# Performance work log

Hardware: AMD Instinct MI355X
Metric: run time of the kernel (lower is better)

Reference implementation:

```python
import jax, jax.numpy as jnp
import numpy as np

L, B, S, E, H, FF = 4, 1, 2048, 768, 12, 3072
DH = E // H
EPS = 1e-5

def setup_inputs() -> dict:
    key = jax.random.key(0)
    ks = jax.random.split(key, 10)
    w = lambda k, shape: jax.random.normal(k, shape, jnp.float32) * 0.02
    return {
        "inputs_embeds": jax.random.normal(ks[0], (B, S, E), jnp.float32),
        "wpe": w(ks[1], (S, E)),
        "ln1_g": jnp.ones((L, E), jnp.float32), "ln1_b": jnp.zeros((L, E), jnp.float32),
        "Wq": w(ks[2], (L, E, E)), "bq": jnp.zeros((L, E), jnp.float32),
        "Wk": w(ks[3], (L, E, E)), "bk": jnp.zeros((L, E), jnp.float32),
        "Wv": w(ks[4], (L, E, E)), "bv": jnp.zeros((L, E), jnp.float32),
        "Wo": w(ks[5], (L, E, E)), "bo": jnp.zeros((L, E), jnp.float32),
        "ln2_g": jnp.ones((L, E), jnp.float32), "ln2_b": jnp.zeros((L, E), jnp.float32),
        "W1": w(ks[6], (L, E, FF)), "b1": jnp.zeros((L, FF), jnp.float32),
        "W2": w(ks[7], (L, FF, E)), "b2": jnp.zeros((L, E), jnp.float32),
        "lnf_g": jnp.ones((E,), jnp.float32), "lnf_b": jnp.zeros((E,), jnp.float32),
    }

def _layernorm(x, g, b):
    mu = jnp.mean(x, axis=-1, keepdims=True)
    var = jnp.mean(jnp.square(x - mu), axis=-1, keepdims=True)
    return (x - mu) * jax.lax.rsqrt(var + EPS) * g + b

def _block(x, p):
    (g1, b1_, wq, bq, wk, bk, wv, bv, wo, bo, g2, b2_, w1, bb1, w2, bb2) = p
    h = _layernorm(x, g1, b1_)
    Bq, Sq, _ = x.shape
    q = (h @ wq + bq).reshape(Bq, Sq, H, DH)
    k = (h @ wk + bk).reshape(Bq, Sq, H, DH)
    v = (h @ wv + bv).reshape(Bq, Sq, H, DH)
    scale = DH ** (-0.5)
    # no softmax: purely linear scale * Q K^T V (attn_weights unused downstream)
    attn_w = jnp.einsum('bqhd,bkhd->bhqk', q, k) * scale  # [B,H,S,S]
    a = jnp.einsum('bhqk,bkhd->bqhd', attn_w, v).reshape(Bq, Sq, E)
    x = x + (a @ wo + bo)
    h2 = _layernorm(x, g2, b2_)
    mlp = jax.nn.gelu(h2 @ w1 + bb1, approximate=False) @ w2 + bb2
    return x + mlp

def reference(inputs_embeds, wpe, ln1_g, ln1_b, Wq, bq, Wk, bk, Wv, bv, Wo, bo,
              ln2_g, ln2_b, W1, b1, W2, b2, lnf_g, lnf_b):
    seq = inputs_embeds.shape[1]
    x = inputs_embeds + wpe[:seq]  # dropout p=0 -> identity
    layer_params = (ln1_g, ln1_b, Wq, bq, Wk, bk, Wv, bv, Wo, bo,
                    ln2_g, ln2_b, W1, b1, W2, b2)
    def body(carry, p):
        return _block(carry, p), None
    x, _ = jax.lax.scan(body, x, layer_params)
    return _layernorm(x, lnf_g, lnf_b)
```

## Files before the change

### kernel.cpp

```cpp
#include <hip/hip_runtime.h>
#include <hip/hip_bf16.h>
#include <math.h>

#define SS 2048
#define EE 768
#define HH 12
#define DHH 64
#define FFF 3072
#define LL 4

typedef __hip_bfloat16 bf16;
typedef __attribute__((ext_vector_type(8))) short short8;
typedef __attribute__((ext_vector_type(4))) float f32x4;

__device__ __forceinline__ float b2f(short u) {
  union { unsigned int i; float f; } v;
  v.i = ((unsigned int)(unsigned short)u) << 16;
  return v.f;
}
__device__ __forceinline__ bf16 f2b(float f) { return __float2bfloat16(f); }
__device__ __forceinline__ unsigned int f2bu(float f) {
  return (unsigned int)__bfloat16_as_ushort(__float2bfloat16(f));
}

__device__ __forceinline__ void async_ld16(const void* g, void* l) {
  __builtin_amdgcn_global_load_lds(
      (const __attribute__((address_space(1))) void*)g,
      (__attribute__((address_space(3))) void*)l, 16, 0, 0);
}

template <typename OutT>
__global__ __launch_bounds__(256) void ln_fused_kernel(
    float* x, const float* __restrict__ bias, const float* __restrict__ part,
    int nparts, const float* __restrict__ extra,
    const float* __restrict__ g, const float* __restrict__ bta,
    int writeback, int readx, OutT* __restrict__ out) {
  int row = blockIdx.x;
  int tid = threadIdx.x;
  float* xr = x + (size_t)row * EE;
  float v0 = 0.f, v1 = 0.f, v2 = 0.f;
  if (readx) { v0 = xr[tid]; v1 = xr[tid + 256]; v2 = xr[tid + 512]; }
  if (bias) { v0 += bias[tid]; v1 += bias[tid + 256]; v2 += bias[tid + 512]; }
  for (int p = 0; p < nparts; p++) {
    const float* pr = part + (size_t)p * SS * EE + (size_t)row * EE;
    v0 += pr[tid]; v1 += pr[tid + 256]; v2 += pr[tid + 512];
  }
  if (extra) {
    const float* er = extra + (size_t)row * EE;
    v0 += er[tid]; v1 += er[tid + 256]; v2 += er[tid + 512];
  }
  if (writeback) { xr[tid] = v0; xr[tid + 256] = v1; xr[tid + 512] = v2; }
  float s  = v0 + v1 + v2;
  float s2 = v0 * v0 + v1 * v1 + v2 * v2;
  #pragma unroll
  for (int off = 32; off >= 1; off >>= 1) {
    s  += __shfl_down(s,  off);
    s2 += __shfl_down(s2, off);
  }
  __shared__ float red[8];
  __shared__ float mb[2];
  int lane = tid & 63, wid = tid >> 6;
  if (lane == 0) { red[wid] = s; red[4 + wid] = s2; }
  __syncthreads();
  if (tid == 0) {
    float ts  = red[0] + red[1] + red[2] + red[3];
    float ts2 = red[4] + red[5] + red[6] + red[7];
    float mu  = ts * (1.0f / EE);
    float var = ts2 * (1.0f / EE) - mu * mu;
    mb[0] = mu; mb[1] = rsqrtf(var + 1e-5f);
  }
  __syncthreads();
  float mu = mb[0], rs = mb[1];
  OutT* orow = out + (size_t)row * EE;
  float o0 = (v0 - mu) * rs * g[tid]       + bta[tid];
  float o1 = (v1 - mu) * rs * g[tid + 256] + bta[tid + 256];
  float o2 = (v2 - mu) * rs * g[tid + 512] + bta[tid + 512];
  if constexpr (sizeof(OutT) == 4) {
    orow[tid] = o0; orow[tid + 256] = o1; orow[tid + 512] = o2;
  } else {
    orow[tid] = f2b(o0); orow[tid + 256] = f2b(o1); orow[tid + 512] = f2b(o2);
  }
}

__global__ __launch_bounds__(256) void transpose_all_kernel(
    const float* __restrict__ Wq, const float* __restrict__ Wk,
    const float* __restrict__ Wv, const float* __restrict__ Wo,
    const float* __restrict__ W1, const float* __restrict__ W2,
    bf16* __restrict__ WtAll) {
  __shared__ unsigned int lds[32][33];
  int bid = blockIdx.x;
  int l = bid / 3456, r = bid % 3456;
  bf16* base = WtAll + (size_t)l * 7077888;
  const float* src; bf16* dst; int K, N, rr;
  if (r < 864) {
    int m = r / 288; rr = r % 288;
    src = (m == 0 ? Wq : m == 1 ? Wk : Wv) + (size_t)l * EE * EE;
    dst = base + (size_t)m * 589824; K = 768; N = 768;
  } else if (r < 1152) {
    rr = r - 864; src = Wo + (size_t)l * EE * EE; dst = base + 1769472; K = 768; N = 768;
  } else if (r < 2304) {
    rr = r - 1152; src = W1 + (size_t)l * EE * FFF; dst = base + 2359296; K = 768; N = 3072;
  } else {
    rr = r - 2304; src = W2 + (size_t)l * FFF * EE; dst = base + 4718592; K = 3072; N = 768;
  }
  int ntn = N >> 5;
  int k0 = (rr / ntn) * 64, n0 = (rr % ntn) * 32;
  int tx = threadIdx.x & 31, ty = threadIdx.x >> 5;
  const float* s = src + (size_t)(k0 + ty * 8) * N + n0 + tx;
  #pragma unroll
  for (int j = 0; j < 4; j++) {
    float v0 = s[(size_t)(2 * j) * N];
    float v1 = s[(size_t)(2 * j + 1) * N];
    lds[tx][ty * 4 + j] = (f2bu(v1) << 16) | f2bu(v0);
  }
  __syncthreads();
  int n = threadIdx.x >> 3, kp4 = (threadIdx.x & 7) * 4;
  uint4 o;
  o.x = lds[n][kp4];     o.y = lds[n][kp4 + 1];
  o.z = lds[n][kp4 + 2]; o.w = lds[n][kp4 + 3];
  unsigned int* d = (unsigned int*)dst + (size_t)(n0 + n) * (K >> 1) + (k0 >> 1) + kp4;
  *(uint4*)d = o;
}

__global__ __launch_bounds__(256) void concat_bias_all_kernel(
    const float* __restrict__ bq, const float* __restrict__ bk,
    const float* __restrict__ bv, float* __restrict__ out) {
  int g = blockIdx.x * 256 + threadIdx.x;
  int l = g / 2304, i = g % 2304;
  out[g] = (i < 768) ? bq[l * 768 + i]
         : (i < 1536 ? bk[l * 768 + i - 768] : bv[l * 768 + i - 1536]);
}

__global__ __launch_bounds__(256) void gemm_bf16_kernel(
    const bf16* __restrict__ A, int lda, const bf16* __restrict__ Bt,
    const float* __restrict__ bias, void* __restrict__ Cv, void* __restrict__ Cv2,
    int K, int N, int mode) {
  __shared__ __align__(16) short As[64 * 64];
  __shared__ __align__(16) short Bs[64 * 64];
  const int t = threadIdx.x;
  const int wave = t >> 6, lane = t & 63;
  const int m0 = blockIdx.y * 64, n0 = blockIdx.x * 64;

  const int srow = t >> 3;
  const int sw   = (t & 7) ^ (srow & 7);
  const bf16* Ag = A  + (size_t)(m0 + srow) * lda + sw * 8;
  const bf16* Bg = Bt + (size_t)(n0 + srow) * K + sw * 8;

  const int fr = lane & 15, kq = lane >> 4;
  const int wm = (wave >> 1) * 32, wn = (wave & 1) * 32;
  f32x4 acc[2][2] = {};

  for (int k0 = 0; k0 < K; k0 += 64) {
    async_ld16(Ag + k0,                    As + wave * 512);
    async_ld16(Ag + (size_t)32 * lda + k0, As + 2048 + wave * 512);
    async_ld16(Bg + k0,                    Bs + wave * 512);
    async_ld16(Bg + (size_t)32 * K + k0,   Bs + 2048 + wave * 512);
    __syncthreads();
    #pragma unroll
    for (int s = 0; s < 2; s++) {
      short8 a[2], b[2];
      #pragma unroll
      for (int i = 0; i < 2; i++) {
        int r = wm + 16 * i + fr;
        int p = (kq + 4 * s) ^ (r & 7);
        a[i] = *(const short8*)(As + r * 64 + p * 8);
      }
      #pragma unroll
      for (int j = 0; j < 2; j++) {
        int r = wn + 16 * j + fr;
        int p = (kq + 4 * s) ^ (r & 7);
        b[j] = *(const short8*)(Bs + r * 64 + p * 8);
      }
      #pragma unroll
      for (int i = 0; i < 2; i++)
        #pragma unroll
        for (int j = 0; j < 2; j++)
          acc[i][j] = __builtin_amdgcn_mfma_f32_16x16x32_bf16(a[i], b[j], acc[i][j], 0, 0, 0);
    }
    __syncthreads();
  }

  #pragma unroll
  for (int i = 0; i < 2; i++) {
    #pragma unroll
    for (int j = 0; j < 2; j++) {
      const int r0 = m0 + wm + 16 * i + kq * 4;
      const int c  = n0 + wn + 16 * j + fr;
      const float bv = bias[c];
      if (mode == 4) {
        if (n0 < 768) {
          #pragma unroll
          for (int ri = 0; ri < 4; ri++)
            ((bf16*)Cv)[(size_t)(r0 + ri) * 768 + c] = f2b(acc[i][j][ri] + bv);
        } else {
          __align__(8) bf16 tb[4];
          #pragma unroll
          for (int ri = 0; ri < 4; ri++) tb[ri] = f2b(acc[i][j][ri] + bv);
          *(short4*)((short*)Cv2 + ((size_t)(c - 768) << 11) + r0) = *(short4*)&tb[0];
        }
      } else {
        #pragma unroll
        for (int ri = 0; ri < 4; ri++) {
          float val = acc[i][j][ri] + bv;
          val = 0.5f * val * (1.0f + erff(val * 0.70710678118654752f));
          ((bf16*)Cv)[(size_t)(r0 + ri) * N + c] = f2b(val);
        }
      }
    }
  }
}

__global__ __launch_bounds__(256) void gemm_resid_kernel(
    const bf16* __restrict__ A, int lda, const bf16* __restrict__ Bt,
    const float* __restrict__ bias, float* __restrict__ x,
    float* __restrict__ part, int K, int zsplit, int Ksplit) {
  __shared__ __align__(16) short As[64 * 64];
  __shared__ __align__(16) short Bs[64 * 64];
  const int t = threadIdx.x;
  const int wave = t >> 6, lane = t & 63;
  const int m0 = blockIdx.y * 64, n0 = blockIdx.x * 64;
  const int z = blockIdx.z;
  const int kBeg = z * Ksplit, kEnd = kBeg + Ksplit;

  const int srow = t >> 3;
  const int sw   = (t & 7) ^ (srow & 7);
  const bf16* Ag = A  + (size_t)(m0 + srow) * lda + sw * 8;
  const bf16* Bg = Bt + (size_t)(n0 + srow) * K + sw * 8;

  const int fr = lane & 15, kq = lane >> 4;
  const int wm = (wave >> 1) * 32, wn = (wave & 1) * 32;
  f32x4 acc[2][2] = {};

  for (int k0 = kBeg; k0 < kEnd; k0 += 64) {
    async_ld16(Ag + k0,                    As + wave * 512);
    async_ld16(Ag + (size_t)32 * lda + k0, As + 2048 + wave * 512);
    async_ld16(Bg + k0,                    Bs + wave * 512);
    async_ld16(Bg + (size_t)32 * K + k0,   Bs + 2048 + wave * 512);
    __syncthreads();
    #pragma unroll
    for (int s = 0; s < 2; s++) {
      short8 a[2], b[2];
      #pragma unroll
      for (int i = 0; i < 2; i++) {
        int r = wm + 16 * i + fr;
        int p = (kq + 4 * s) ^ (r & 7);
        a[i] = *(const short8*)(As + r * 64 + p * 8);
      }
      #pragma unroll
      for (int j = 0; j < 2; j++) {
        int r = wn + 16 * j + fr;
        int p = (kq + 4 * s) ^ (r & 7);
        b[j] = *(const short8*)(Bs + r * 64 + p * 8);
      }
      #pragma unroll
      for (int i = 0; i < 2; i++)
        #pragma unroll
        for (int j = 0; j < 2; j++)
          acc[i][j] = __builtin_amdgcn_mfma_f32_16x16x32_bf16(a[i], b[j], acc[i][j], 0, 0, 0);
    }
    __syncthreads();
  }

  #pragma unroll
  for (int i = 0; i < 2; i++) {
    #pragma unroll
    for (int j = 0; j < 2; j++) {
      const int r0 = m0 + wm + 16 * i + kq * 4;
      const int c  = n0 + wn + 16 * j + fr;
      if (zsplit > 1) {
        #pragma unroll
        for (int ri = 0; ri < 4; ri++)
          part[(size_t)z * SS * EE + (size_t)(r0 + ri) * EE + c] = acc[i][j][ri];
      } else {
        const float bv = bias[c];
        #pragma unroll
        for (int ri = 0; ri < 4; ri++) {
          const size_t idx = (size_t)(r0 + ri) * EE + c;
          x[idx] = acc[i][j][ri] + bv + x[idx];
        }
      }
    }
  }
}

__global__ __launch_bounds__(256) void attn_fused_kernel(
    const bf16* __restrict__ kvT, const bf16* __restrict__ Wo_t,
    bf16* __restrict__ Gt) {
  __shared__ short pbuf[4][4096];
  __shared__ short Ms[4096];
  const int nt = blockIdx.x, h = blockIdx.y;
  const int lane = threadIdx.x & 63, wave = threadIdx.x >> 6;
  const int fr = lane & 15, kq = lane >> 4;
  const short* kT = (const short*)kvT + (size_t)h * 64 * 2048;
  const short* vT = (const short*)kvT + (size_t)(768 + h * 64) * 2048;

  f32x4 acc[4][4] = {};
  for (int it = 0; it < 8; it++) {
    const int s0 = (it * 4 + wave) * 64;
    #pragma unroll
    for (int s = 0; s < 2; s++) {
      short8 a[4], b[4];
      #pragma unroll
      for (int i = 0; i < 4; i++)
        a[i] = *(const short8*)(kT + (size_t)(16 * i + fr) * 2048 + s0 + s * 32 + kq * 8);
      #pragma unroll
      for (int j = 0; j < 4; j++)
        b[j] = *(const short8*)(vT + (size_t)(16 * j + fr) * 2048 + s0 + s * 32 + kq * 8);
      #pragma unroll
      for (int i = 0; i < 4; i++)
        #pragma unroll
        for (int j = 0; j < 4; j++)
          acc[i][j] = __builtin_amdgcn_mfma_f32_16x16x32_bf16(a[i], b[j], acc[i][j], 0, 0, 0);
    }
  }
  #pragma unroll
  for (int i = 0; i < 4; i++)
    #pragma unroll
    for (int j = 0; j < 4; j++)
      #pragma unroll
      for (int ri = 0; ri < 4; ri++)
        pbuf[wave][(16 * i + kq * 4 + ri) * 64 + 16 * j + fr] =
            (short)__bfloat16_as_ushort(f2b(acc[i][j][ri]));
  __syncthreads();
  {
    int e0 = threadIdx.x * 16;
    #pragma unroll
    for (int e = 0; e < 16; e++) {
      float s = b2f(pbuf[0][e0 + e]) + b2f(pbuf[1][e0 + e]) +
                b2f(pbuf[2][e0 + e]) + b2f(pbuf[3][e0 + e]);
      Ms[e0 + e] = (short)__bfloat16_as_ushort(f2b(s * 0.125f));
    }
  }
  __syncthreads();

  const int nb = nt * 128 + wave * 32;
  f32x4 g[4][2] = {};
  #pragma unroll
  for (int s = 0; s < 2; s++) {
    short8 a[4], b[2];
    #pragma unroll
    for (int i = 0; i < 4; i++)
      a[i] = *(const short8*)(Ms + (16 * i + fr) * 64 + s * 32 + kq * 8);
    #pragma unroll
    for (int j = 0; j < 2; j++)
      b[j] = *(const short8*)((const short*)Wo_t +
             (size_t)(nb + 16 * j + fr) * 768 + h * 64 + s * 32 + kq * 8);
    #pragma unroll
    for (int i = 0; i < 4; i++)
      #pragma unroll
      for (int j = 0; j < 2; j++)
        g[i][j] = __builtin_amdgcn_mfma_f32_16x16x32_bf16(a[i], b[j], g[i][j], 0, 0, 0);
  }
  #pragma unroll
  for (int i = 0; i < 4; i++)
    #pragma unroll
    for (int j = 0; j < 2; j++) {
      const int c = nb + 16 * j + fr;
      const int d1 = 16 * i + kq * 4;
      __align__(8) bf16 tb[4];
      #pragma unroll
      for (int ri = 0; ri < 4; ri++) tb[ri] = f2b(g[i][j][ri]);
      *(short4*)((short*)Gt + (size_t)c * 768 + h * 64 + d1) = *(short4*)&tb[0];
    }
}

extern "C" void kernel_launch(void* const* d_in, const int* in_sizes, int n_in,
                              void* d_out, int out_size, void* d_ws, size_t ws_size,
                              hipStream_t stream) {
  const float* emb  = (const float*)d_in[0];
  const float* wpe  = (const float*)d_in[1];
  const float* ln1g = (const float*)d_in[2];
  const float* ln1b = (const float*)d_in[3];
  const float* Wq   = (const float*)d_in[4];
  const float* bq   = (const float*)d_in[5];
  const float* Wk   = (const float*)d_in[6];
  const float* bk   = (const float*)d_in[7];
  const float* Wv   = (const float*)d_in[8];
  const float* bv   = (const float*)d_in[9];
  const float* Wo   = (const float*)d_in[10];
  const float* bo   = (const float*)d_in[11];
  const float* ln2g = (const float*)d_in[12];
  const float* ln2b = (const float*)d_in[13];
  const float* W1   = (const float*)d_in[14];
  const float* b1   = (const float*)d_in[15];
  const float* W2   = (const float*)d_in[16];
  const float* b2   = (const float*)d_in[17];
  const float* lnfg = (const float*)d_in[18];
  const float* lnfb = (const float*)d_in[19];

  char* w = (char*)d_ws;
  bf16*  WtAll = (bf16*)w;   w += (size_t)4 * 7077888 * 2;
  float* bqkvA = (float*)w;  w += (size_t)4 * 2304 * 4;
  float* x     = (float*)w;  w += (size_t)SS * EE * 4;
  bf16*  hb    = (bf16*)w;   w += (size_t)SS * EE * 2;
  bf16*  qkvQ  = (bf16*)w;   w += (size_t)SS * EE * 2;
  bf16*  kvT   = (bf16*)w;   w += (size_t)1536 * 2048 * 2;
  bf16*  Gt    = (bf16*)w;   w += (size_t)EE * EE * 2;
  bf16*  mb2   = (bf16*)w;   w += (size_t)SS * FFF * 2;
  float* cpart = (float*)w;  w += (size_t)2 * SS * EE * 4;

  dim3 blk(256);
  transpose_all_kernel<<<13824, blk, 0, stream>>>(Wq, Wk, Wv, Wo, W1, W2, WtAll);
  concat_bias_all_kernel<<<36, blk, 0, stream>>>(bq, bk, bv, bqkvA);

  for (int l = 0; l < LL; l++) {
    bf16* Wl = WtAll + (size_t)l * 7077888;
    bf16* Wqkv_t = Wl;
    bf16* Wo_t   = Wl + 1769472;
    bf16* W1_t   = Wl + 2359296;
    bf16* W2_t   = Wl + 4718592;

    if (l == 0) {
      ln_fused_kernel<bf16><<<SS, blk, 0, stream>>>(
          x, nullptr, emb, 1, wpe, ln1g, ln1b, 1, 0, hb);
    } else {
      ln_fused_kernel<bf16><<<SS, blk, 0, stream>>>(
          x, b2 + (l - 1) * EE, cpart, 2, nullptr,
          ln1g + l * EE, ln1b + l * EE, 1, 1, hb);
    }
    gemm_bf16_kernel<<<dim3(36, 32), blk, 0, stream>>>(
        hb, EE, Wqkv_t, bqkvA + l * 2304, qkvQ, kvT, EE, 2304, 4);
    attn_fused_kernel<<<dim3(6, HH), blk, 0, stream>>>(kvT, Wo_t, Gt);
    gemm_resid_kernel<<<dim3(12, 32), blk, 0, stream>>>(
        qkvQ, EE, Gt, bo + l * EE, x, nullptr, EE, 1, EE);
    ln_fused_kernel<bf16><<<SS, blk, 0, stream>>>(
        x, nullptr, nullptr, 0, nullptr, ln2g + l * EE, ln2b + l * EE, 0, 1, hb);
    gemm_bf16_kernel<<<dim3(48, 32), blk, 0, stream>>>(
        hb, EE, W1_t, b1 + l * FFF, mb2, nullptr, EE, FFF, 1);
    gemm_resid_kernel<<<dim3(12, 32, 2), blk, 0, stream>>>(
        mb2, FFF, W2_t, nullptr, nullptr, cpart, FFF, 2, 1536);
  }
  ln_fused_kernel<float><<<SS, blk, 0, stream>>>(
      x, b2 + 3 * EE, cpart, 2, nullptr, lnfg, lnfb, 0, 1, (float*)d_out);
}
```

Baseline: 595.7 us.

## Use 128x128 GEMM tiles for QKV/FFN and split-K by four for W2

Replaces the 64x64 tile GEMM with a 128x128 tile kernel (4x4 MFMA fragments per wave) for the QKV, W1 and W2 projections. This raises arithmetic intensity and cuts LDS and global reloads per output. The W2 GEMM now splits K four ways into a larger partial buffer, which the following layernorm sums. The weight-transpose kernel also switches to float4 loads. Larger tiles mean fewer blocks (288 or 384 for QKV/W1) on a 256-CU part, plus more register pressure, so occupancy and wave balance may suffer.

```diff
diff --git a/kernel.cpp b/kernel.cpp
--- a/kernel.cpp
+++ b/kernel.cpp
@@ -105,21 +105,21 @@
   }
   int ntn = N >> 5;
   int k0 = (rr / ntn) * 64, n0 = (rr % ntn) * 32;
-  int tx = threadIdx.x & 31, ty = threadIdx.x >> 5;
-  const float* s = src + (size_t)(k0 + ty * 8) * N + n0 + tx;
-  #pragma unroll
-  for (int j = 0; j < 4; j++) {
-    float v0 = s[(size_t)(2 * j) * N];
-    float v1 = s[(size_t)(2 * j + 1) * N];
-    lds[tx][ty * 4 + j] = (f2bu(v1) << 16) | f2bu(v0);
-  }
+  int kp = threadIdx.x >> 3, ns = (threadIdx.x & 7) * 4;
+  const float* s0 = src + (size_t)(k0 + 2 * kp) * N + n0 + ns;
+  float4 e = *(const float4*)s0;
+  float4 o = *(const float4*)(s0 + N);
+  lds[ns + 0][kp] = (f2bu(o.x) << 16) | f2bu(e.x);
+  lds[ns + 1][kp] = (f2bu(o.y) << 16) | f2bu(e.y);
+  lds[ns + 2][kp] = (f2bu(o.z) << 16) | f2bu(e.z);
+  lds[ns + 3][kp] = (f2bu(o.w) << 16) | f2bu(e.w);
   __syncthreads();
   int n = threadIdx.x >> 3, kp4 = (threadIdx.x & 7) * 4;
-  uint4 o;
-  o.x = lds[n][kp4];     o.y = lds[n][kp4 + 1];
-  o.z = lds[n][kp4 + 2]; o.w = lds[n][kp4 + 3];
+  uint4 ov;
+  ov.x = lds[n][kp4];     ov.y = lds[n][kp4 + 1];
+  ov.z = lds[n][kp4 + 2]; ov.w = lds[n][kp4 + 3];
   unsigned int* d = (unsigned int*)dst + (size_t)(n0 + n) * (K >> 1) + (k0 >> 1) + kp4;
-  *(uint4*)d = o;
+  *(uint4*)d = ov;
 }
 
 __global__ __launch_bounds__(256) void concat_bias_all_kernel(
@@ -131,15 +131,15 @@
          : (i < 1536 ? bk[l * 768 + i - 768] : bv[l * 768 + i - 1536]);
 }
 
-__global__ __launch_bounds__(256) void gemm_bf16_kernel(
+__global__ __launch_bounds__(256) void gemm128_kernel(
     const bf16* __restrict__ A, int lda, const bf16* __restrict__ Bt,
     const float* __restrict__ bias, void* __restrict__ Cv, void* __restrict__ Cv2,
-    int K, int N, int mode) {
-  __shared__ __align__(16) short As[64 * 64];
-  __shared__ __align__(16) short Bs[64 * 64];
+    float* __restrict__ part, int K, int N, int mode, int Ksplit) {
+  __shared__ __align__(16) short As[128 * 64];
+  __shared__ __align__(16) short Bs[128 * 64];
   const int t = threadIdx.x;
   const int wave = t >> 6, lane = t & 63;
-  const int m0 = blockIdx.y * 64, n0 = blockIdx.x * 64;
+  const int m0 = blockIdx.y * 128, n0 = blockIdx.x * 128;
 
   const int srow = t >> 3;
   const int sw   = (t & 7) ^ (srow & 7);
@@ -147,47 +147,56 @@
   const bf16* Bg = Bt + (size_t)(n0 + srow) * K + sw * 8;
 
   const int fr = lane & 15, kq = lane >> 4;
-  const int wm = (wave >> 1) * 32, wn = (wave & 1) * 32;
-  f32x4 acc[2][2] = {};
-
-  for (int k0 = 0; k0 < K; k0 += 64) {
-    async_ld16(Ag + k0,                    As + wave * 512);
-    async_ld16(Ag + (size_t)32 * lda + k0, As + 2048 + wave * 512);
-    async_ld16(Bg + k0,                    Bs + wave * 512);
-    async_ld16(Bg + (size_t)32 * K + k0,   Bs + 2048 + wave * 512);
+  const int wm = (wave >> 1) * 64, wn = (wave & 1) * 64;
+  f32x4 acc[4][4] = {};
+
+  int kBeg = 0, kEnd = K;
+  if (mode == 2) { kBeg = blockIdx.z * Ksplit; kEnd = kBeg + Ksplit; }
+
+  for (int k0 = kBeg; k0 < kEnd; k0 += 64) {
+    #pragma unroll
+    for (int q = 0; q < 4; q++) {
+      async_ld16(Ag + (size_t)(q * 32) * lda + k0, As + q * 2048 + wave * 512);
+      async_ld16(Bg + (size_t)(q * 32) * K  + k0, Bs + q * 2048 + wave * 512);
+    }
     __syncthreads();
     #pragma unroll
     for (int s = 0; s < 2; s++) {
-      short8 a[2], b[2];
-      #pragma unroll
-      for (int i = 0; i < 2; i++) {
+      short8 a[4], b[4];
+      #pragma unroll
+      for (int i = 0; i < 4; i++) {
         int r = wm + 16 * i + fr;
         int p = (kq + 4 * s) ^ (r & 7);
         a[i] = *(const short8*)(As + r * 64 + p * 8);
       }
       #pragma unroll
-      for (int j = 0; j < 2; j++) {
+      for (int j = 0; j < 4; j++) {
         int r = wn + 16 * j + fr;
         int p = (kq + 4 * s) ^ (r & 7);
         b[j] = *(const short8*)(Bs + r * 64 + p * 8);
       }
       #pragma unroll
-      for (int i = 0; i < 2; i++)
+      for (int i = 0; i < 4; i++)
         #pragma unroll
-        for (int j = 0; j < 2; j++)
+        for (int j = 0; j < 4; j++)
           acc[i][j] = __builtin_amdgcn_mfma_f32_16x16x32_bf16(a[i], b[j], acc[i][j], 0, 0, 0);
     }
     __syncthreads();
   }
 
   #pragma unroll
-  for (int i = 0; i < 2; i++) {
-    #pragma unroll
-    for (int j = 0; j < 2; j++) {
+  for (int i = 0; i < 4; i++) {
+    #pragma unroll
+    for (int j = 0; j < 4; j++) {
       const int r0 = m0 + wm + 16 * i + kq * 4;
       const int c  = n0 + wn + 16 * j + fr;
-      const float bv = bias[c];
-      if (mode == 4) {
+      if (mode == 2) {
+        #pragma unroll
+        for (int ri = 0; ri < 4; ri++)
+          part[(size_t)blockIdx.z * SS * EE + (size_t)(r0 + ri) * EE + c] =
+              acc[i][j][ri];
+      } else if (mode == 4) {
+        const float bv = bias[c];
         if (n0 < 768) {
           #pragma unroll
           for (int ri = 0; ri < 4; ri++)
@@ -199,6 +208,7 @@
           *(short4*)((short*)Cv2 + ((size_t)(c - 768) << 11) + r0) = *(short4*)&tb[0];
         }
       } else {
+        const float bv = bias[c];
         #pragma unroll
         for (int ri = 0; ri < 4; ri++) {
           float val = acc[i][j][ri] + bv;
@@ -212,15 +222,12 @@
 
 __global__ __launch_bounds__(256) void gemm_resid_kernel(
     const bf16* __restrict__ A, int lda, const bf16* __restrict__ Bt,
-    const float* __restrict__ bias, float* __restrict__ x,
-    float* __restrict__ part, int K, int zsplit, int Ksplit) {
+    const float* __restrict__ bias, float* __restrict__ x, int K) {
   __shared__ __align__(16) short As[64 * 64];
   __shared__ __align__(16) short Bs[64 * 64];
   const int t = threadIdx.x;
   const int wave = t >> 6, lane = t & 63;
   const int m0 = blockIdx.y * 64, n0 = blockIdx.x * 64;
-  const int z = blockIdx.z;
-  const int kBeg = z * Ksplit, kEnd = kBeg + Ksplit;
 
   const int srow = t >> 3;
   const int sw   = (t & 7) ^ (srow & 7);
@@ -231,7 +238,7 @@
   const int wm = (wave >> 1) * 32, wn = (wave & 1) * 32;
   f32x4 acc[2][2] = {};
 
-  for (int k0 = kBeg; k0 < kEnd; k0 += 64) {
+  for (int k0 = 0; k0 < K; k0 += 64) {
     async_ld16(Ag + k0,                    As + wave * 512);
     async_ld16(Ag + (size_t)32 * lda + k0, As + 2048 + wave * 512);
     async_ld16(Bg + k0,                    Bs + wave * 512);
@@ -267,17 +274,11 @@
     for (int j = 0; j < 2; j++) {
       const int r0 = m0 + wm + 16 * i + kq * 4;
       const int c  = n0 + wn + 16 * j + fr;
-      if (zsplit > 1) {
-        #pragma unroll
-        for (int ri = 0; ri < 4; ri++)
-          part[(size_t)z * SS * EE + (size_t)(r0 + ri) * EE + c] = acc[i][j][ri];
-      } else {
-        const float bv = bias[c];
-        #pragma unroll
-        for (int ri = 0; ri < 4; ri++) {
-          const size_t idx = (size_t)(r0 + ri) * EE + c;
-          x[idx] = acc[i][j][ri] + bv + x[idx];
-        }
+      const float bv = bias[c];
+      #pragma unroll
+      for (int ri = 0; ri < 4; ri++) {
+        const size_t idx = (size_t)(r0 + ri) * EE + c;
+        x[idx] = acc[i][j][ri] + bv + x[idx];
       }
     }
   }
@@ -397,7 +398,7 @@
   bf16*  kvT   = (bf16*)w;   w += (size_t)1536 * 2048 * 2;
   bf16*  Gt    = (bf16*)w;   w += (size_t)EE * EE * 2;
   bf16*  mb2   = (bf16*)w;   w += (size_t)SS * FFF * 2;
-  float* cpart = (float*)w;  w += (size_t)2 * SS * EE * 4;
+  float* cpart = (float*)w;  w += (size_t)4 * SS * EE * 4;
 
   dim3 blk(256);
   transpose_all_kernel<<<13824, blk, 0, stream>>>(Wq, Wk, Wv, Wo, W1, W2, WtAll);
@@ -415,21 +416,21 @@
           x, nullptr, emb, 1, wpe, ln1g, ln1b, 1, 0, hb);
     } else {
       ln_fused_kernel<bf16><<<SS, blk, 0, stream>>>(
-          x, b2 + (l - 1) * EE, cpart, 2, nullptr,
+          x, b2 + (l - 1) * EE, cpart, 4, nullptr,
           ln1g + l * EE, ln1b + l * EE, 1, 1, hb);
     }
-    gemm_bf16_kernel<<<dim3(36, 32), blk, 0, stream>>>(
-        hb, EE, Wqkv_t, bqkvA + l * 2304, qkvQ, kvT, EE, 2304, 4);
+    gemm128_kernel<<<dim3(18, 16), blk, 0, stream>>>(
+        hb, EE, Wqkv_t, bqkvA + l * 2304, qkvQ, kvT, nullptr, EE, 2304, 4, 0);
     attn_fused_kernel<<<dim3(6, HH), blk, 0, stream>>>(kvT, Wo_t, Gt);
     gemm_resid_kernel<<<dim3(12, 32), blk, 0, stream>>>(
-        qkvQ, EE, Gt, bo + l * EE, x, nullptr, EE, 1, EE);
+        qkvQ, EE, Gt, bo + l * EE, x, EE);
     ln_fused_kernel<bf16><<<SS, blk, 0, stream>>>(
         x, nullptr, nullptr, 0, nullptr, ln2g + l * EE, ln2b + l * EE, 0, 1, hb);
-    gemm_bf16_kernel<<<dim3(48, 32), blk, 0, stream>>>(
-        hb, EE, W1_t, b1 + l * FFF, mb2, nullptr, EE, FFF, 1);
-    gemm_resid_kernel<<<dim3(12, 32, 2), blk, 0, stream>>>(
-        mb2, FFF, W2_t, nullptr, nullptr, cpart, FFF, 2, 1536);
+    gemm128_kernel<<<dim3(24, 16), blk, 0, stream>>>(
+        hb, EE, W1_t, b1 + l * FFF, mb2, nullptr, nullptr, EE, FFF, 1, 0);
+    gemm128_kernel<<<dim3(6, 16, 4), blk, 0, stream>>>(
+        mb2, FFF, W2_t, nullptr, nullptr, nullptr, cpart, FFF, EE, 2, 768);
   }
   ln_fused_kernel<float><<<SS, blk, 0, stream>>>(
-      x, b2 + 3 * EE, cpart, 2, nullptr, lnfg, lnfb, 0, 1, (float*)d_out);
-}
+      x, b2 + 3 * EE, cpart, 4, nullptr, lnfg, lnfb, 0, 1, (float*)d_out);
+}
```

After: 656.3 us. +10.2%, slower.
